# Optimization experiments

Measured on AMD Instinct MI355X. Metric: run time of the kernel, lower is better.

## Reference

```python
import jax, jax.numpy as jnp
import numpy as np

B, N, M, D = 8, 1024, 2048, 1024


def setup_inputs() -> dict:
    key = jax.random.key(0)
    k1, k2, k3 = jax.random.split(key, 3)
    text_features = jax.random.normal(k1, (B, N, D), dtype=jnp.float32)
    audio_features = jax.random.normal(k2, (B, M, D), dtype=jnp.float32)
    sigma = jnp.ones((1,), dtype=jnp.float32)  # learnable bandwidth, initial_sigma=1.0
    # audio lengths in [M//4, M) so no softmax row is fully masked
    audio_lengths = jnp.maximum(
        jax.random.randint(k3, (B,), 0, M), M // 4
    ).astype(jnp.int32)
    return {
        "text_features": text_features,
        "audio_features": audio_features,
        "sigma": sigma,
        "audio_lengths": audio_lengths,
    }


def reference(text_features, audio_features, sigma, audio_lengths):
    b, n, d = text_features.shape
    m = audio_features.shape[1]
    s = jnp.abs(sigma[0]) + 1e-8

    # QK^T / sqrt(d)  -> (B, N, M)
    scores = jnp.einsum("bnd,bmd->bnm", text_features, audio_features) / jnp.sqrt(
        jnp.float32(d)
    )

    # Gaussian relative positional bias: -|i/N - j/M|^2 / (2 sigma^2)
    text_pos = jnp.arange(n, dtype=jnp.float32) / n    # (N,)
    audio_pos = jnp.arange(m, dtype=jnp.float32) / m   # (M,)
    d_rel = jnp.abs(text_pos[:, None] - audio_pos[None, :])  # (N, M)
    scores = scores - d_rel**2 / (2.0 * s * s)

    # mask padded audio positions per batch element
    valid = jnp.arange(m)[None, :] < audio_lengths[:, None]  # (B, M) bool
    scores = jnp.where(valid[:, None, :], scores, -jnp.inf)

    attention_weights = jax.nn.softmax(scores, axis=-1)  # (B, N, M)
    enhanced = jnp.einsum("bnm,bmd->bnd", attention_weights, audio_features)
    return enhanced, attention_weights
```

## Files before the change

kernel.cpp:

```cpp
#include <hip/hip_runtime.h>
#include <hip/hip_bf16.h>

#define BB 8
#define NN 1024
#define MM 2048
#define DD 1024

typedef __attribute__((ext_vector_type(8))) __bf16 bfrag8;
typedef __attribute__((ext_vector_type(4))) float ffrag4;

__device__ __forceinline__ unsigned short f2bf(float f) {
  union { float f; unsigned u; } x; x.f = f;
  unsigned r = x.u + 0x7FFFu + ((x.u >> 16) & 1u);
  return (unsigned short)(r >> 16);
}

__device__ __forceinline__ void gload_lds16(const unsigned short* g, unsigned short* l) {
  __builtin_amdgcn_global_load_lds(
      (const __attribute__((address_space(1))) void*)g,
      (__attribute__((address_space(3))) void*)l, 16, 0, 0);
}

#define SCHED0() __builtin_amdgcn_sched_barrier(0)
#define P_PRE()  do { SCHED0(); __builtin_amdgcn_s_barrier();                 \
                      asm volatile("s_waitcnt lgkmcnt(0)" ::: "memory");      \
                      SCHED0(); __builtin_amdgcn_s_setprio(1); } while (0)
#define P_POST() do { __builtin_amdgcn_s_setprio(0); SCHED0();                \
                      __builtin_amdgcn_s_barrier(); } while (0)

#define MFMA16x16x32 __builtin_amdgcn_mfma_f32_16x16x32_bf16

__device__ __forceinline__ void stage_half(const unsigned short* gbase, int ldk,
                                           unsigned short* ldst,
                                           int w, int r0, int slog) {
  const unsigned short* g = gbase + (size_t)(w * 8 + r0) * ldk + slog;
  gload_lds16(g, ldst + w * 512);
  gload_lds16(g + (size_t)64 * ldk, ldst + 4096 + w * 512);
}

#define TSTR 68
__global__ __launch_bounds__(256) void ta_prep(
    const float* __restrict__ Q, const float* __restrict__ V,
    unsigned short* __restrict__ Qbf,
    unsigned short* __restrict__ Kbf, unsigned short* __restrict__ VT,
    float* __restrict__ sums)
{
  __shared__ unsigned short Tls[64 * TSTR];
  const int bid = blockIdx.x;
  const int t = threadIdx.x;

  if (bid < 4096) {
    int tt = bid * 256 + t;
    const float4* src = reinterpret_cast<const float4*>(Q) + tt * 2;
    float4 a = src[0], b = src[1];
    ushort4 lo = { f2bf(a.x), f2bf(a.y), f2bf(a.z), f2bf(a.w) };
    ushort4 hi = { f2bf(b.x), f2bf(b.y), f2bf(b.z), f2bf(b.w) };
    ushort4* dst = reinterpret_cast<ushort4*>(Qbf) + tt * 2;
    dst[0] = lo; dst[1] = hi;
  } else if (bid < 8192) {
    const int id = bid - 4096;
    const int dt = id & 15;
    const int mt = (id >> 4) & 31;
    const int b  = id >> 9;

    const float* Vb = V + (size_t)b * MM * DD + (size_t)(mt * 64) * DD + dt * 64;
#pragma unroll
    for (int it = 0; it < 4; ++it) {
      int slot = t + 256 * it;
      int row  = slot >> 4;
      int c4   = slot & 15;
      float4 a = *reinterpret_cast<const float4*>(Vb + (size_t)row * DD + c4 * 4);
      ushort4 h = { f2bf(a.x), f2bf(a.y), f2bf(a.z), f2bf(a.w) };
      *reinterpret_cast<ushort4*>(&Tls[row * TSTR + c4 * 4]) = h;
    }
    __syncthreads();

    unsigned short* Kb = Kbf + (size_t)b * MM * DD + (size_t)(mt * 64) * DD + dt * 64;
    unsigned short* Vt = VT  + (size_t)b * DD * MM + (size_t)(dt * 64) * MM + mt * 64;
#pragma unroll
    for (int it = 0; it < 4; ++it) {
      int slot = t + 256 * it;
      int row  = slot >> 4;
      int c4   = slot & 15;
      *reinterpret_cast<ushort4*>(Kb + (size_t)row * DD + c4 * 4) =
          *reinterpret_cast<const ushort4*>(&Tls[row * TSTR + c4 * 4]);
      ushort4 tv = { Tls[(c4 * 4 + 0) * TSTR + row],
                     Tls[(c4 * 4 + 1) * TSTR + row],
                     Tls[(c4 * 4 + 2) * TSTR + row],
                     Tls[(c4 * 4 + 3) * TSTR + row] };
      *reinterpret_cast<ushort4*>(Vt + (size_t)row * MM + c4 * 4) = tv;
    }
  } else {
    int tt = (bid - 8192) * 256 + t;
    sums[tt] = 0.0f;
  }
}

__global__ void ta_zero(float* __restrict__ sums) {
  int t = blockIdx.x * 256 + threadIdx.x;
  if (t < BB * NN) sums[t] = 0.0f;
}

__global__ __launch_bounds__(512, 2) void ta_gemm1x(
    const unsigned short* __restrict__ Q,
    const unsigned short* __restrict__ K,
    const float* __restrict__ sigma,
    const int* __restrict__ lens,
    unsigned short* __restrict__ Ebf,
    float* __restrict__ rowsum)
{
  const int bj = blockIdx.x, bi = blockIdx.y, b = blockIdx.z;
  const int t = threadIdx.x;
  const int lane = t & 63, w = t >> 6;
  const int wr = w >> 2, wc = w & 3;
  __shared__ unsigned short S[65536];

  const unsigned short* Qb = Q + (size_t)b * NN * DD + (size_t)(bi * 256) * DD;
  const unsigned short* Kb = K + (size_t)b * MM * DD + (size_t)(bj * 256) * DD;

  const int r  = lane & 15, qd = lane >> 4;
  const int r0 = (lane >> 3) & 7;
  const int slog = ((lane & 7) ^ r0) << 3;
  const int cs0 = ((qd)     ^ (r & 7)) << 3;
  const int cs1 = ((4 + qd) ^ (r & 7)) << 3;

  ffrag4 acc[8][4] = {};

  {
    unsigned short* T0 = &S[0];
    stage_half(Qb,                        DD, T0,          w, r0, slog);
    stage_half(Qb + (size_t)128 * DD,     DD, T0 + 8192,   w, r0, slog);
    stage_half(Kb,                        DD, T0 + 16384,  w, r0, slog);
    stage_half(Kb + (size_t)128 * DD,     DD, T0 + 24576,  w, r0, slog);
    unsigned short* T1 = &S[32768];
    stage_half(Qb + 64,                    DD, T1,          w, r0, slog);
    stage_half(Qb + (size_t)128 * DD + 64, DD, T1 + 8192,   w, r0, slog);
    stage_half(Kb + 64,                    DD, T1 + 16384,  w, r0, slog);
    stage_half(Kb + (size_t)128 * DD + 64, DD, T1 + 24576,  w, r0, slog);
    asm volatile("s_waitcnt vmcnt(8)" ::: "memory");
    __builtin_amdgcn_s_barrier();
  }

  for (int kt = 0; kt < 16; ++kt) {
    const int p = kt & 1;
    unsigned short* Ab = &S[p * 32768 + wr * 8192];
    unsigned short* Bb = &S[p * 32768 + 16384 + (wc >> 1) * 8192];
    const int brb = (wc & 1) * 64;
    bfrag8 af[4][2], bf0[2][2], bf1[2][2];

#pragma unroll
    for (int mi = 0; mi < 4; ++mi) {
      const unsigned short* a = &Ab[(mi * 16 + r) * 64];
      af[mi][0] = *reinterpret_cast<const bfrag8*>(a + cs0);
      af[mi][1] = *reinterpret_cast<const bfrag8*>(a + cs1);
    }
#pragma unroll
    for (int jj = 0; jj < 2; ++jj) {
      const unsigned short* bp = &Bb[(brb + jj * 16 + r) * 64];
      bf0[jj][0] = *reinterpret_cast<const bfrag8*>(bp + cs0);
      bf0[jj][1] = *reinterpret_cast<const bfrag8*>(bp + cs1);
    }
    P_PRE();
#pragma unroll
    for (int mi = 0; mi < 4; ++mi)
#pragma unroll
      for (int jj = 0; jj < 2; ++jj) {
        acc[mi][jj] = MFMA16x16x32(af[mi][0], bf0[jj][0], acc[mi][jj], 0, 0, 0);
        acc[mi][jj] = MFMA16x16x32(af[mi][1], bf0[jj][1], acc[mi][jj], 0, 0, 0);
      }
    P_POST();

#pragma unroll
    for (int jj = 0; jj < 2; ++jj) {
      const unsigned short* bp = &Bb[(brb + (2 + jj) * 16 + r) * 64];
      bf1[jj][0] = *reinterpret_cast<const bfrag8*>(bp + cs0);
      bf1[jj][1] = *reinterpret_cast<const bfrag8*>(bp + cs1);
    }
    P_PRE();
#pragma unroll
    for (int mi = 0; mi < 4; ++mi)
#pragma unroll
      for (int jj = 0; jj < 2; ++jj) {
        acc[mi][2 + jj] = MFMA16x16x32(af[mi][0], bf1[jj][0], acc[mi][2 + jj], 0, 0, 0);
        acc[mi][2 + jj] = MFMA16x16x32(af[mi][1], bf1[jj][1], acc[mi][2 + jj], 0, 0, 0);
      }
    P_POST();

#pragma unroll
    for (int mi = 0; mi < 4; ++mi) {
      const unsigned short* a = &Ab[((mi + 4) * 16 + r) * 64];
      af[mi][0] = *reinterpret_cast<const bfrag8*>(a + cs0);
      af[mi][1] = *reinterpret_cast<const bfrag8*>(a + cs1);
    }
    if (kt + 2 < 16) {
      unsigned short* Dst = &S[p * 32768 + 16384];
      stage_half(Kb + (kt + 2) * 64,                    DD, Dst,        w, r0, slog);
      stage_half(Kb + (size_t)128 * DD + (kt + 2) * 64, DD, Dst + 8192, w, r0, slog);
    }
    P_PRE();
#pragma unroll
    for (int mi = 0; mi < 4; ++mi)
#pragma unroll
      for (int jj = 0; jj < 2; ++jj) {
        acc[4 + mi][2 + jj] = MFMA16x16x32(af[mi][0], bf1[jj][0], acc[4 + mi][2 + jj], 0, 0, 0);
        acc[4 + mi][2 + jj] = MFMA16x16x32(af[mi][1], bf1[jj][1], acc[4 + mi][2 + jj], 0, 0, 0);
      }
    P_POST();

    if (kt + 2 < 16) {
      unsigned short* Dst = &S[p * 32768];
      stage_half(Qb + (kt + 2) * 64,                    DD, Dst,        w, r0, slog);
      stage_half(Qb + (size_t)128 * DD + (kt + 2) * 64, DD, Dst + 8192, w, r0, slog);
    }
    P_PRE();
#pragma unroll
    for (int mi = 0; mi < 4; ++mi)
#pragma unroll
      for (int jj = 0; jj < 2; ++jj) {
        acc[4 + mi][jj] = MFMA16x16x32(af[mi][0], bf0[jj][0], acc[4 + mi][jj], 0, 0, 0);
        acc[4 + mi][jj] = MFMA16x16x32(af[mi][1], bf0[jj][1], acc[4 + mi][jj], 0, 0, 0);
      }
    __builtin_amdgcn_s_setprio(0);
    SCHED0();
    if (kt + 2 < 16)      { asm volatile("s_waitcnt vmcnt(8)" ::: "memory"); }
    else if (kt + 1 < 16) { asm volatile("s_waitcnt vmcnt(0)" ::: "memory"); }
    __builtin_amdgcn_s_barrier();
  }

  const float sg = fabsf(sigma[0]) + 1e-8f;
  const float inv2s2 = 1.0f / (2.0f * sg * sg);
  const int len = lens[b];
  unsigned short* Erow = Ebf + (size_t)b * NN * MM;
  float* sums = rowsum + (size_t)b * NN;
  const int ibase = bi * 256 + wr * 128;
  const int jbase = bj * 256 + wc * 64;
#pragma unroll
  for (int mi = 0; mi < 8; ++mi) {
#pragma unroll
    for (int v = 0; v < 4; ++v) {
      int i = ibase + mi * 16 + qd * 4 + v;
      float psum = 0.0f;
#pragma unroll
      for (int nj = 0; nj < 4; ++nj) {
        int j = jbase + nj * 16 + r;
        float e = 0.0f;
        if (j < len) {
          float dr = (float)i * (1.0f / (float)NN) - (float)j * (1.0f / (float)MM);
          float sc = acc[mi][nj][v] * 0.03125f - dr * dr * inv2s2;
          e = __expf(fminf(sc, 30.0f));
        }
        psum += e;
        Erow[(size_t)i * MM + j] = f2bf(e);
      }
      psum += __shfl_xor(psum, 1);
      psum += __shfl_xor(psum, 2);
      psum += __shfl_xor(psum, 4);
      psum += __shfl_xor(psum, 8);
      if (r == 0) atomicAdd(&sums[i], psum);
    }
  }
}

__global__ __launch_bounds__(512, 2) void ta_gemm2x(
    const unsigned short* __restrict__ E,
    const unsigned short* __restrict__ VT,
    const float* __restrict__ rowsum,
    float* __restrict__ O,
    float* __restrict__ attn)
{
  const int bd = blockIdx.x, bi = blockIdx.y, b = blockIdx.z;
  const int t = threadIdx.x;
  const int lane = t & 63, w = t >> 6;
  const int wr = w >> 2, wc = w & 3;
  __shared__ unsigned short S[49152];

  const unsigned short* Eb = E  + (size_t)b * NN * MM + (size_t)(bi * 128) * MM;
  const unsigned short* Vb = VT + (size_t)b * DD * MM + (size_t)(bd * 256) * MM;

  const int r  = lane & 15, qd = lane >> 4;
  const int r0 = (lane >> 3) & 7;
  const int slog = ((lane & 7) ^ r0) << 3;
  const int cs0 = ((qd)     ^ (r & 7)) << 3;
  const int cs1 = ((4 + qd) ^ (r & 7)) << 3;

  ffrag4 acc[4][4] = {};

  {
    stage_half(Eb,                        MM, &S[0],     w, r0, slog);
    stage_half(Vb,                        MM, &S[8192],  w, r0, slog);
    stage_half(Vb + (size_t)128 * MM,     MM, &S[16384], w, r0, slog);
    stage_half(Eb + 64,                    MM, &S[24576],         w, r0, slog);
    stage_half(Vb + 64,                    MM, &S[24576 + 8192],  w, r0, slog);
    stage_half(Vb + (size_t)128 * MM + 64, MM, &S[24576 + 16384], w, r0, slog);
    asm volatile("s_waitcnt vmcnt(6)" ::: "memory");
    __builtin_amdgcn_s_barrier();
  }

  for (int kt = 0; kt < 32; ++kt) {
    const int p = kt & 1;
    unsigned short* Ab = &S[p * 24576];
    unsigned short* Bb = &S[p * 24576 + 8192 + (wc >> 1) * 8192];
    const int arb = wr * 64;
    const int brb = (wc & 1) * 64;
    bfrag8 af[2][2], bf0[2][2], bf1[2][2];

#pragma unroll
    for (int mi = 0; mi < 2; ++mi) {
      const unsigned short* a = &Ab[(arb + mi * 16 + r) * 64];
      af[mi][0] = *reinterpret_cast<const bfrag8*>(a + cs0);
      af[mi][1] = *reinterpret_cast<const bfrag8*>(a + cs1);
    }
#pragma unroll
    for (int jj = 0; jj < 2; ++jj) {
      const unsigned short* bp = &Bb[(brb + jj * 16 + r) * 64];
      bf0[jj][0] = *reinterpret_cast<const bfrag8*>(bp + cs0);
      bf0[jj][1] = *reinterpret_cast<const bfrag8*>(bp + cs1);
    }
    P_PRE();
#pragma unroll
    for (int mi = 0; mi < 2; ++mi)
#pragma unroll
      for (int jj = 0; jj < 2; ++jj) {
        acc[mi][jj] = MFMA16x16x32(af[mi][0], bf0[jj][0], acc[mi][jj], 0, 0, 0);
        acc[mi][jj] = MFMA16x16x32(af[mi][1], bf0[jj][1], acc[mi][jj], 0, 0, 0);
      }
    P_POST();

#pragma unroll
    for (int jj = 0; jj < 2; ++jj) {
      const unsigned short* bp = &Bb[(brb + (2 + jj) * 16 + r) * 64];
      bf1[jj][0] = *reinterpret_cast<const bfrag8*>(bp + cs0);
      bf1[jj][1] = *reinterpret_cast<const bfrag8*>(bp + cs1);
    }
    P_PRE();
#pragma unroll
    for (int mi = 0; mi < 2; ++mi)
#pragma unroll
      for (int jj = 0; jj < 2; ++jj) {
        acc[mi][2 + jj] = MFMA16x16x32(af[mi][0], bf1[jj][0], acc[mi][2 + jj], 0, 0, 0);
        acc[mi][2 + jj] = MFMA16x16x32(af[mi][1], bf1[jj][1], acc[mi][2 + jj], 0, 0, 0);
      }
    P_POST();

#pragma unroll
    for (int mi = 0; mi < 2; ++mi) {
      const unsigned short* a = &Ab[(arb + (mi + 2) * 16 + r) * 64];
      af[mi][0] = *reinterpret_cast<const bfrag8*>(a + cs0);
      af[mi][1] = *reinterpret_cast<const bfrag8*>(a + cs1);
    }
    if (kt + 2 < 32) {
      unsigned short* Dst = &S[p * 24576 + 8192];
      stage_half(Vb + (kt + 2) * 64,                    MM, Dst,        w, r0, slog);
      stage_half(Vb + (size_t)128 * MM + (kt + 2) * 64, MM, Dst + 8192, w, r0, slog);
    }
    P_PRE();
#pragma unroll
    for (int mi = 0; mi < 2; ++mi)
#pragma unroll
      for (int jj = 0; jj < 2; ++jj) {
        acc[2 + mi][2 + jj] = MFMA16x16x32(af[mi][0], bf1[jj][0], acc[2 + mi][2 + jj], 0, 0, 0);
        acc[2 + mi][2 + jj] = MFMA16x16x32(af[mi][1], bf1[jj][1], acc[2 + mi][2 + jj], 0, 0, 0);
      }
    P_POST();

    if (kt + 2 < 32) {
      stage_half(Eb + (kt + 2) * 64, MM, &S[p * 24576], w, r0, slog);
    }
    P_PRE();
#pragma unroll
    for (int mi = 0; mi < 2; ++mi)
#pragma unroll
      for (int jj = 0; jj < 2; ++jj) {
        acc[2 + mi][jj] = MFMA16x16x32(af[mi][0], bf0[jj][0], acc[2 + mi][jj], 0, 0, 0);
        acc[2 + mi][jj] = MFMA16x16x32(af[mi][1], bf0[jj][1], acc[2 + mi][jj], 0, 0, 0);
      }
    __builtin_amdgcn_s_setprio(0);
    SCHED0();
    if (kt + 2 < 32)      { asm volatile("s_waitcnt vmcnt(6)" ::: "memory"); }
    else if (kt + 1 < 32) { asm volatile("s_waitcnt vmcnt(0)" ::: "memory"); }
    __builtin_amdgcn_s_barrier();
  }

  float* Ob = O + (size_t)b * NN * DD;
  const float* rs = rowsum + (size_t)b * NN;
  const int ibase = bi * 128 + wr * 64;
  const int dbase = bd * 256 + wc * 64;
#pragma unroll
  for (int mi = 0; mi < 4; ++mi) {
#pragma unroll
    for (int v = 0; v < 4; ++v) {
      int i = ibase + mi * 16 + qd * 4 + v;
      float inv = 1.0f / fmaxf(rs[i], 1e-30f);
#pragma unroll
      for (int nj = 0; nj < 4; ++nj) {
        int d = dbase + nj * 16 + r;
        Ob[(size_t)i * DD + d] = acc[mi][nj][v] * inv;
      }
    }
  }

  {
    float* attnB = attn + ((size_t)b * NN + bi * 128) * MM + bd * 512;
    const unsigned short* Eslice = Eb + bd * 512;
#pragma unroll
    for (int it = 0; it < 16; ++it) {
      int c = t + it * 512;
      int row = c >> 6;
      int col = (c & 63) * 8;
      float inv = 1.0f / fmaxf(rs[bi * 128 + row], 1e-30f);
      uint4 x = *reinterpret_cast<const uint4*>(Eslice + (size_t)row * MM + col);
      unsigned u[4] = { x.x, x.y, x.z, x.w };
      float o[8];
#pragma unroll
      for (int k = 0; k < 4; ++k) {
        union { unsigned u; float f; } lo, hi;
        lo.u = u[k] << 16; hi.u = u[k] & 0xFFFF0000u;
        o[2 * k]     = lo.f * inv;
        o[2 * k + 1] = hi.f * inv;
      }
      float4* dst = reinterpret_cast<float4*>(attnB + (size_t)row * MM + col);
      float4 f0 = { o[0], o[1], o[2], o[3] };
      float4 f1 = { o[4], o[5], o[6], o[7] };
      dst[0] = f0; dst[1] = f1;
    }
  }
}

#define LDA 40
__global__ __launch_bounds__(256) void tb_gemm1e(
    const float* __restrict__ Q, const float* __restrict__ K,
    const float* __restrict__ sigma, const int* __restrict__ lens,
    float* __restrict__ attn, float* __restrict__ rowsum)
{
  const int bj = blockIdx.x, bi = blockIdx.y, b = blockIdx.z;
  const int t = threadIdx.x;
  const int lane = t & 63;
  const int w = t >> 6;
  const int wi = w >> 1, wj = w & 1;
  __shared__ unsigned short Als[128 * LDA];
  __shared__ unsigned short Bls[128 * LDA];
  const float* Qb = Q + (size_t)b * NN * DD + (size_t)(bi * 128) * DD;
  const float* Kb = K + (size_t)b * MM * DD + (size_t)(bj * 128) * DD;
  ffrag4 acc[4][4] = {};
  const int r = lane & 15;
  const int koff = (lane >> 4) * 8;
  for (int k0 = 0; k0 < DD; k0 += 32) {
#pragma unroll
    for (int it = 0; it < 4; ++it) {
      int slot = t + 256 * it;
      int row = slot >> 3, c4 = slot & 7;
      float4 qa = *reinterpret_cast<const float4*>(Qb + (size_t)row * DD + k0 + c4 * 4);
      float4 ka = *reinterpret_cast<const float4*>(Kb + (size_t)row * DD + k0 + c4 * 4);
      ushort4 qh = { f2bf(qa.x), f2bf(qa.y), f2bf(qa.z), f2bf(qa.w) };
      ushort4 kh = { f2bf(ka.x), f2bf(ka.y), f2bf(ka.z), f2bf(ka.w) };
      *reinterpret_cast<ushort4*>(&Als[row * LDA + c4 * 4]) = qh;
      *reinterpret_cast<ushort4*>(&Bls[row * LDA + c4 * 4]) = kh;
    }
    __syncthreads();
    bfrag8 af[4], bf[4];
#pragma unroll
    for (int ti = 0; ti < 4; ++ti)
      af[ti] = *reinterpret_cast<const bfrag8*>(&Als[(wi * 64 + ti * 16 + r) * LDA + koff]);
#pragma unroll
    for (int tj = 0; tj < 4; ++tj)
      bf[tj] = *reinterpret_cast<const bfrag8*>(&Bls[(wj * 64 + tj * 16 + r) * LDA + koff]);
#pragma unroll
    for (int ti = 0; ti < 4; ++ti)
#pragma unroll
      for (int tj = 0; tj < 4; ++tj)
        acc[ti][tj] = MFMA16x16x32(af[ti], bf[tj], acc[ti][tj], 0, 0, 0);
    __syncthreads();
  }
  const float s = fabsf(sigma[0]) + 1e-8f;
  const float inv2s2 = 1.0f / (2.0f * s * s);
  const int len = lens[b];
  float* Prow = attn + (size_t)b * NN * MM;
  float* sums = rowsum + (size_t)b * NN;
  const int ibase = bi * 128 + wi * 64;
  const int jbase = bj * 128 + wj * 64;
  const int quad = lane >> 4;
#pragma unroll
  for (int ti = 0; ti < 4; ++ti) {
#pragma unroll
    for (int v = 0; v < 4; ++v) {
      int i = ibase + ti * 16 + quad * 4 + v;
      float psum = 0.0f;
#pragma unroll
      for (int tj = 0; tj < 4; ++tj) {
        int j = jbase + tj * 16 + r;
        float e = 0.0f;
        if (j < len) {
          float dr = (float)i * (1.0f / (float)NN) - (float)j * (1.0f / (float)MM);
          float sc = acc[ti][tj][v] * 0.03125f - dr * dr * inv2s2;
          e = __expf(fminf(sc, 30.0f));
        }
        psum += e;
        Prow[(size_t)i * MM + j] = e;
      }
      psum += __shfl_xor(psum, 1);
      psum += __shfl_xor(psum, 2);
      psum += __shfl_xor(psum, 4);
      psum += __shfl_xor(psum, 8);
      if (r == 0) atomicAdd(&sums[i], psum);
    }
  }
}

__global__ __launch_bounds__(256) void tb_norm(float* __restrict__ attn,
                                               const float* __restrict__ sums) {
  int t = blockIdx.x * 256 + threadIdx.x;
  int row = t >> 9;
  const float inv = 1.0f / fmaxf(sums[row], 1e-30f);
  float4* p = reinterpret_cast<float4*>(attn) + t;
  float4 x = *p;
  x.x *= inv; x.y *= inv; x.z *= inv; x.w *= inv;
  *p = x;
}

__global__ __launch_bounds__(256) void tb_gemm2(
    const float* __restrict__ P, const float* __restrict__ V, float* __restrict__ O)
{
  const int bd = blockIdx.x, bi = blockIdx.y, b = blockIdx.z;
  const int t = threadIdx.x;
  const int lane = t & 63;
  const int w = t >> 6;
  const int wi = w >> 1, wj = w & 1;
  __shared__ unsigned short Pls[128 * LDA];
  __shared__ unsigned short Vls[128 * LDA];
  const float* Pb = P + (size_t)b * NN * MM + (size_t)(bi * 128) * MM;
  const float* Vb = V + (size_t)b * MM * DD + bd * 128;
  ffrag4 acc[4][4] = {};
  const int r = lane & 15;
  const int koff = (lane >> 4) * 8;
  const int vd = t & 127;
  const int vmb = (t >> 7) * 16;
  for (int k0 = 0; k0 < MM; k0 += 32) {
#pragma unroll
    for (int it = 0; it < 4; ++it) {
      int slot = t + 256 * it;
      int row = slot >> 3, c4 = slot & 7;
      float4 pa = *reinterpret_cast<const float4*>(Pb + (size_t)row * MM + k0 + c4 * 4);
      ushort4 ph = { f2bf(pa.x), f2bf(pa.y), f2bf(pa.z), f2bf(pa.w) };
      *reinterpret_cast<ushort4*>(&Pls[row * LDA + c4 * 4]) = ph;
    }
    union { unsigned short h[16]; uint4 q[2]; } hv;
#pragma unroll
    for (int i = 0; i < 16; ++i)
      hv.h[i] = f2bf(Vb[(size_t)(k0 + vmb + i) * DD + vd]);
    *reinterpret_cast<uint4*>(&Vls[vd * LDA + vmb]) = hv.q[0];
    *reinterpret_cast<uint4*>(&Vls[vd * LDA + vmb + 8]) = hv.q[1];
    __syncthreads();
    bfrag8 af[4], bf[4];
#pragma unroll
    for (int ti = 0; ti < 4; ++ti)
      af[ti] = *reinterpret_cast<const bfrag8*>(&Pls[(wi * 64 + ti * 16 + r) * LDA + koff]);
#pragma unroll
    for (int tj = 0; tj < 4; ++tj)
      bf[tj] = *reinterpret_cast<const bfrag8*>(&Vls[(wj * 64 + tj * 16 + r) * LDA + koff]);
#pragma unroll
    for (int ti = 0; ti < 4; ++ti)
#pragma unroll
      for (int tj = 0; tj < 4; ++tj)
        acc[ti][tj] = MFMA16x16x32(af[ti], bf[tj], acc[ti][tj], 0, 0, 0);
    __syncthreads();
  }
  float* Ob = O + (size_t)b * NN * DD;
  const int ibase = bi * 128 + wi * 64;
  const int dbase = bd * 128 + wj * 64;
#pragma unroll
  for (int ti = 0; ti < 4; ++ti) {
#pragma unroll
    for (int tj = 0; tj < 4; ++tj) {
      int d = dbase + tj * 16 + r;
#pragma unroll
      for (int v = 0; v < 4; ++v) {
        int i = ibase + ti * 16 + (lane >> 4) * 4 + v;
        Ob[(size_t)i * DD + d] = acc[ti][tj][v];
      }
    }
  }
}

extern "C" void kernel_launch(void* const* d_in, const int* in_sizes, int n_in,
                              void* d_out, int out_size, void* d_ws, size_t ws_size,
                              hipStream_t stream) {
  const float* text  = (const float*)d_in[0];
  const float* audio = (const float*)d_in[1];
  const float* sigma = (const float*)d_in[2];
  const int*   lens  = (const int*)d_in[3];

  float* out = (float*)d_out;
  float* enhanced = out;
  float* attn = out + (size_t)BB * NN * DD;

  const size_t QBF  = (size_t)BB * NN * DD * 2;
  const size_t KBF  = (size_t)BB * MM * DD * 2;
  const size_t VTB  = (size_t)BB * DD * MM * 2;
  const size_t EBF  = (size_t)BB * NN * MM * 2;
  const size_t offQ = 65536;
  const size_t offK = offQ + QBF;
  const size_t offV = offK + KBF;
  const size_t offE = offV + VTB;
  const size_t need = offE + EBF;

  float* rowsum = (float*)d_ws;

  if (ws_size >= need) {
    unsigned short* Qbf = (unsigned short*)((char*)d_ws + offQ);
    unsigned short* Kbf = (unsigned short*)((char*)d_ws + offK);
    unsigned short* VT  = (unsigned short*)((char*)d_ws + offV);
    unsigned short* Ebf = (unsigned short*)((char*)d_ws + offE);

    ta_prep<<<dim3(8224), 256, 0, stream>>>(text, audio, Qbf, Kbf, VT, rowsum);
    ta_gemm1x<<<dim3(MM / 256, NN / 256, BB), 512, 0, stream>>>(Qbf, Kbf, sigma, lens, Ebf, rowsum);
    ta_gemm2x<<<dim3(DD / 256, NN / 128, BB), 512, 0, stream>>>(Ebf, VT, rowsum, enhanced, attn);
  } else {
    ta_zero<<<dim3((BB * NN + 255) / 256), 256, 0, stream>>>(rowsum);
    tb_gemm1e<<<dim3(MM / 128, NN / 128, BB), 256, 0, stream>>>(text, audio, sigma, lens, attn, rowsum);
    tb_norm<<<dim3(BB * NN * MM / 4 / 256), 256, 0, stream>>>(attn, rowsum);
    tb_gemm2<<<dim3(DD / 128, NN / 128, BB), 256, 0, stream>>>(attn, audio, enhanced);
  }
}
```

Measured before the change: 276.6 us.

## Interleave attention-weight writeback into PV loop, remap blocks, trim barriers

```diff
diff --git a/kernel.cpp b/kernel.cpp
--- a/kernel.cpp
+++ b/kernel.cpp
@@ -22,12 +22,6 @@
 }
 
 #define SCHED0() __builtin_amdgcn_sched_barrier(0)
-#define P_PRE()  do { SCHED0(); __builtin_amdgcn_s_barrier();                 \
-                      asm volatile("s_waitcnt lgkmcnt(0)" ::: "memory");      \
-                      SCHED0(); __builtin_amdgcn_s_setprio(1); } while (0)
-#define P_POST() do { __builtin_amdgcn_s_setprio(0); SCHED0();                \
-                      __builtin_amdgcn_s_barrier(); } while (0)
-
 #define MFMA16x16x32 __builtin_amdgcn_mfma_f32_16x16x32_bf16
 
 __device__ __forceinline__ void stage_half(const unsigned short* gbase, int ldk,
@@ -109,7 +103,10 @@
     unsigned short* __restrict__ Ebf,
     float* __restrict__ rowsum)
 {
-  const int bj = blockIdx.x, bi = blockIdx.y, b = blockIdx.z;
+  const int lin = blockIdx.x + 8 * (blockIdx.y + 4 * blockIdx.z);
+  const int wid = (lin & 7) * 32 + (lin >> 3);
+  const int bj = wid & 7, bi = (wid >> 3) & 3, b = wid >> 5;
+
   const int t = threadIdx.x;
   const int lane = t & 63, w = t >> 6;
   const int wr = w >> 2, wc = w & 3;
@@ -141,6 +138,7 @@
     __builtin_amdgcn_s_barrier();
   }
 
+#pragma unroll 2
   for (int kt = 0; kt < 16; ++kt) {
     const int p = kt & 1;
     unsigned short* Ab = &S[p * 32768 + wr * 8192];
@@ -160,7 +158,8 @@
       bf0[jj][0] = *reinterpret_cast<const bfrag8*>(bp + cs0);
       bf0[jj][1] = *reinterpret_cast<const bfrag8*>(bp + cs1);
     }
-    P_PRE();
+    asm volatile("s_waitcnt lgkmcnt(0)" ::: "memory");
+    SCHED0(); __builtin_amdgcn_s_setprio(1);
 #pragma unroll
     for (int mi = 0; mi < 4; ++mi)
 #pragma unroll
@@ -168,7 +167,7 @@
         acc[mi][jj] = MFMA16x16x32(af[mi][0], bf0[jj][0], acc[mi][jj], 0, 0, 0);
         acc[mi][jj] = MFMA16x16x32(af[mi][1], bf0[jj][1], acc[mi][jj], 0, 0, 0);
       }
-    P_POST();
+    __builtin_amdgcn_s_setprio(0); SCHED0();
 
 #pragma unroll
     for (int jj = 0; jj < 2; ++jj) {
@@ -176,7 +175,9 @@
       bf1[jj][0] = *reinterpret_cast<const bfrag8*>(bp + cs0);
       bf1[jj][1] = *reinterpret_cast<const bfrag8*>(bp + cs1);
     }
-    P_PRE();
+    asm volatile("s_waitcnt lgkmcnt(0)" ::: "memory");
+    SCHED0(); __builtin_amdgcn_s_barrier();
+    __builtin_amdgcn_s_setprio(1);
 #pragma unroll
     for (int mi = 0; mi < 4; ++mi)
 #pragma unroll
@@ -184,7 +185,7 @@
         acc[mi][2 + jj] = MFMA16x16x32(af[mi][0], bf1[jj][0], acc[mi][2 + jj], 0, 0, 0);
         acc[mi][2 + jj] = MFMA16x16x32(af[mi][1], bf1[jj][1], acc[mi][2 + jj], 0, 0, 0);
       }
-    P_POST();
+    __builtin_amdgcn_s_setprio(0); SCHED0();
 
 #pragma unroll
     for (int mi = 0; mi < 4; ++mi) {
@@ -197,7 +198,9 @@
       stage_half(Kb + (kt + 2) * 64,                    DD, Dst,        w, r0, slog);
       stage_half(Kb + (size_t)128 * DD + (kt + 2) * 64, DD, Dst + 8192, w, r0, slog);
     }
-    P_PRE();
+    asm volatile("s_waitcnt lgkmcnt(0)" ::: "memory");
+    SCHED0(); __builtin_amdgcn_s_barrier();
+    __builtin_amdgcn_s_setprio(1);
 #pragma unroll
     for (int mi = 0; mi < 4; ++mi)
 #pragma unroll
@@ -205,14 +208,14 @@
         acc[4 + mi][2 + jj] = MFMA16x16x32(af[mi][0], bf1[jj][0], acc[4 + mi][2 + jj], 0, 0, 0);
         acc[4 + mi][2 + jj] = MFMA16x16x32(af[mi][1], bf1[jj][1], acc[4 + mi][2 + jj], 0, 0, 0);
       }
-    P_POST();
+    __builtin_amdgcn_s_setprio(0); SCHED0();
 
     if (kt + 2 < 16) {
       unsigned short* Dst = &S[p * 32768];
       stage_half(Qb + (kt + 2) * 64,                    DD, Dst,        w, r0, slog);
       stage_half(Qb + (size_t)128 * DD + (kt + 2) * 64, DD, Dst + 8192, w, r0, slog);
     }
-    P_PRE();
+    SCHED0(); __builtin_amdgcn_s_setprio(1);
 #pragma unroll
     for (int mi = 0; mi < 4; ++mi)
 #pragma unroll
@@ -220,8 +223,7 @@
         acc[4 + mi][jj] = MFMA16x16x32(af[mi][0], bf0[jj][0], acc[4 + mi][jj], 0, 0, 0);
         acc[4 + mi][jj] = MFMA16x16x32(af[mi][1], bf0[jj][1], acc[4 + mi][jj], 0, 0, 0);
       }
-    __builtin_amdgcn_s_setprio(0);
-    SCHED0();
+    __builtin_amdgcn_s_setprio(0); SCHED0();
     if (kt + 2 < 16)      { asm volatile("s_waitcnt vmcnt(8)" ::: "memory"); }
     else if (kt + 1 < 16) { asm volatile("s_waitcnt vmcnt(0)" ::: "memory"); }
     __builtin_amdgcn_s_barrier();
@@ -268,7 +270,10 @@
     float* __restrict__ O,
     float* __restrict__ attn)
 {
-  const int bd = blockIdx.x, bi = blockIdx.y, b = blockIdx.z;
+  const int lin = blockIdx.x + 4 * (blockIdx.y + 8 * blockIdx.z);
+  const int wid = (lin & 7) * 32 + (lin >> 3);
+  const int bd = wid & 3, bi = (wid >> 2) & 7, b = wid >> 5;
+
   const int t = threadIdx.x;
   const int lane = t & 63, w = t >> 6;
   const int wr = w >> 2, wc = w & 3;
@@ -284,6 +289,14 @@
   const int cs1 = ((4 + qd) ^ (r & 7)) << 3;
 
   ffrag4 acc[4][4] = {};
+
+  const float* rsB = rowsum + (size_t)b * NN;
+  const float* rsT = rsB + bi * 128;
+  float* attnB = attn + ((size_t)b * NN + bi * 128) * MM + bd * 512;
+  const unsigned short* Eslice = Eb + bd * 512;
+  uint4 ax = {0, 0, 0, 0};
+  float ainv = 0.0f;
+  int arow = 0, acol = 0;
 
   {
     stage_half(Eb,                        MM, &S[0],     w, r0, slog);
@@ -296,93 +309,86 @@
     __builtin_amdgcn_s_barrier();
   }
 
+#pragma unroll 2
   for (int kt = 0; kt < 32; ++kt) {
     const int p = kt & 1;
     unsigned short* Ab = &S[p * 24576];
     unsigned short* Bb = &S[p * 24576 + 8192 + (wc >> 1) * 8192];
     const int arb = wr * 64;
     const int brb = (wc & 1) * 64;
-    bfrag8 af[2][2], bf0[2][2], bf1[2][2];
-
-#pragma unroll
-    for (int mi = 0; mi < 2; ++mi) {
+    bfrag8 af[4][2], bf[4][2];
+
+#pragma unroll
+    for (int mi = 0; mi < 4; ++mi) {
       const unsigned short* a = &Ab[(arb + mi * 16 + r) * 64];
       af[mi][0] = *reinterpret_cast<const bfrag8*>(a + cs0);
       af[mi][1] = *reinterpret_cast<const bfrag8*>(a + cs1);
     }
 #pragma unroll
-    for (int jj = 0; jj < 2; ++jj) {
-      const unsigned short* bp = &Bb[(brb + jj * 16 + r) * 64];
-      bf0[jj][0] = *reinterpret_cast<const bfrag8*>(bp + cs0);
-      bf0[jj][1] = *reinterpret_cast<const bfrag8*>(bp + cs1);
-    }
-    P_PRE();
+    for (int nj = 0; nj < 4; ++nj) {
+      const unsigned short* bp = &Bb[(brb + nj * 16 + r) * 64];
+      bf[nj][0] = *reinterpret_cast<const bfrag8*>(bp + cs0);
+      bf[nj][1] = *reinterpret_cast<const bfrag8*>(bp + cs1);
+    }
+
+    if ((kt & 1) == 0) {
+      int it = kt >> 1;
+      int c = t + it * 512;
+      arow = c >> 6;
+      acol = (c & 63) * 8;
+      ax = *reinterpret_cast<const uint4*>(Eslice + (size_t)arow * MM + acol);
+      ainv = 1.0f / fmaxf(rsT[arow], 1e-30f);
+    } else {
+      unsigned u[4] = { ax.x, ax.y, ax.z, ax.w };
+      float o[8];
+#pragma unroll
+      for (int k2 = 0; k2 < 4; ++k2) {
+        union { unsigned u; float f; } lo, hi;
+        lo.u = u[k2] << 16; hi.u = u[k2] & 0xFFFF0000u;
+        o[2 * k2]     = lo.f * ainv;
+        o[2 * k2 + 1] = hi.f * ainv;
+      }
+      float4* dst = reinterpret_cast<float4*>(attnB + (size_t)arow * MM + acol);
+      float4 f0 = { o[0], o[1], o[2], o[3] };
+      float4 f1 = { o[4], o[5], o[6], o[7] };
+      dst[0] = f0; dst[1] = f1;
+    }
+
+    asm volatile("s_waitcnt lgkmcnt(0)" ::: "memory");
+    SCHED0(); __builtin_amdgcn_s_barrier();
+    __builtin_amdgcn_s_setprio(1);
 #pragma unroll
     for (int mi = 0; mi < 2; ++mi)
 #pragma unroll
-      for (int jj = 0; jj < 2; ++jj) {
-        acc[mi][jj] = MFMA16x16x32(af[mi][0], bf0[jj][0], acc[mi][jj], 0, 0, 0);
-        acc[mi][jj] = MFMA16x16x32(af[mi][1], bf0[jj][1], acc[mi][jj], 0, 0, 0);
-      }
-    P_POST();
-
-#pragma unroll
-    for (int jj = 0; jj < 2; ++jj) {
-      const unsigned short* bp = &Bb[(brb + (2 + jj) * 16 + r) * 64];
-      bf1[jj][0] = *reinterpret_cast<const bfrag8*>(bp + cs0);
-      bf1[jj][1] = *reinterpret_cast<const bfrag8*>(bp + cs1);
-    }
-    P_PRE();
-#pragma unroll
-    for (int mi = 0; mi < 2; ++mi)
-#pragma unroll
-      for (int jj = 0; jj < 2; ++jj) {
-        acc[mi][2 + jj] = MFMA16x16x32(af[mi][0], bf1[jj][0], acc[mi][2 + jj], 0, 0, 0);
-        acc[mi][2 + jj] = MFMA16x16x32(af[mi][1], bf1[jj][1], acc[mi][2 + jj], 0, 0, 0);
-      }
-    P_POST();
-
-#pragma unroll
-    for (int mi = 0; mi < 2; ++mi) {
-      const unsigned short* a = &Ab[(arb + (mi + 2) * 16 + r) * 64];
-      af[mi][0] = *reinterpret_cast<const bfrag8*>(a + cs0);
-      af[mi][1] = *reinterpret_cast<const bfrag8*>(a + cs1);
-    }
+      for (int nj = 0; nj < 4; ++nj) {
+        acc[mi][nj] = MFMA16x16x32(af[mi][0], bf[nj][0], acc[mi][nj], 0, 0, 0);
+        acc[mi][nj] = MFMA16x16x32(af[mi][1], bf[nj][1], acc[mi][nj], 0, 0, 0);
+      }
+    __builtin_amdgcn_s_setprio(0); SCHED0();
+
     if (kt + 2 < 32) {
-      unsigned short* Dst = &S[p * 24576 + 8192];
-      stage_half(Vb + (kt + 2) * 64,                    MM, Dst,        w, r0, slog);
-      stage_half(Vb + (size_t)128 * MM + (kt + 2) * 64, MM, Dst + 8192, w, r0, slog);
-    }
-    P_PRE();
-#pragma unroll
-    for (int mi = 0; mi < 2; ++mi)
-#pragma unroll
-      for (int jj = 0; jj < 2; ++jj) {
-        acc[2 + mi][2 + jj] = MFMA16x16x32(af[mi][0], bf1[jj][0], acc[2 + mi][2 + jj], 0, 0, 0);
-        acc[2 + mi][2 + jj] = MFMA16x16x32(af[mi][1], bf1[jj][1], acc[2 + mi][2 + jj], 0, 0, 0);
-      }
-    P_POST();
-
-    if (kt + 2 < 32) {
-      stage_half(Eb + (kt + 2) * 64, MM, &S[p * 24576], w, r0, slog);
-    }
-    P_PRE();
-#pragma unroll
-    for (int mi = 0; mi < 2; ++mi)
-#pragma unroll
-      for (int jj = 0; jj < 2; ++jj) {
-        acc[2 + mi][jj] = MFMA16x16x32(af[mi][0], bf0[jj][0], acc[2 + mi][jj], 0, 0, 0);
-        acc[2 + mi][jj] = MFMA16x16x32(af[mi][1], bf0[jj][1], acc[2 + mi][jj], 0, 0, 0);
-      }
-    __builtin_amdgcn_s_setprio(0);
-    SCHED0();
+      unsigned short* Dst = &S[p * 24576];
+      stage_half(Eb + (kt + 2) * 64,                    MM, Dst,         w, r0, slog);
+      stage_half(Vb + (kt + 2) * 64,                    MM, Dst + 8192,  w, r0, slog);
+      stage_half(Vb + (size_t)128 * MM + (kt + 2) * 64, MM, Dst + 16384, w, r0, slog);
+    }
+
+    SCHED0(); __builtin_amdgcn_s_setprio(1);
+#pragma unroll
+    for (int mi = 2; mi < 4; ++mi)
+#pragma unroll
+      for (int nj = 0; nj < 4; ++nj) {
+        acc[mi][nj] = MFMA16x16x32(af[mi][0], bf[nj][0], acc[mi][nj], 0, 0, 0);
+        acc[mi][nj] = MFMA16x16x32(af[mi][1], bf[nj][1], acc[mi][nj], 0, 0, 0);
+      }
+    __builtin_amdgcn_s_setprio(0); SCHED0();
+
     if (kt + 2 < 32)      { asm volatile("s_waitcnt vmcnt(6)" ::: "memory"); }
     else if (kt + 1 < 32) { asm volatile("s_waitcnt vmcnt(0)" ::: "memory"); }
     __builtin_amdgcn_s_barrier();
   }
 
   float* Ob = O + (size_t)b * NN * DD;
-  const float* rs = rowsum + (size_t)b * NN;
   const int ibase = bi * 128 + wr * 64;
   const int dbase = bd * 256 + wc * 64;
 #pragma unroll
@@ -390,38 +396,12 @@
 #pragma unroll
     for (int v = 0; v < 4; ++v) {
       int i = ibase + mi * 16 + qd * 4 + v;
-      float inv = 1.0f / fmaxf(rs[i], 1e-30f);
+      float inv = 1.0f / fmaxf(rsB[i], 1e-30f);
 #pragma unroll
       for (int nj = 0; nj < 4; ++nj) {
         int d = dbase + nj * 16 + r;
         Ob[(size_t)i * DD + d] = acc[mi][nj][v] * inv;
       }
-    }
-  }
-
-  {
-    float* attnB = attn + ((size_t)b * NN + bi * 128) * MM + bd * 512;
-    const unsigned short* Eslice = Eb + bd * 512;
-#pragma unroll
-    for (int it = 0; it < 16; ++it) {
-      int c = t + it * 512;
-      int row = c >> 6;
-      int col = (c & 63) * 8;
-      float inv = 1.0f / fmaxf(rs[bi * 128 + row], 1e-30f);
-      uint4 x = *reinterpret_cast<const uint4*>(Eslice + (size_t)row * MM + col);
-      unsigned u[4] = { x.x, x.y, x.z, x.w };
-      float o[8];
-#pragma unroll
-      for (int k = 0; k < 4; ++k) {
-        union { unsigned u; float f; } lo, hi;
-        lo.u = u[k] << 16; hi.u = u[k] & 0xFFFF0000u;
-        o[2 * k]     = lo.f * inv;
-        o[2 * k + 1] = hi.f * inv;
-      }
-      float4* dst = reinterpret_cast<float4*>(attnB + (size_t)row * MM + col);
-      float4 f0 = { o[0], o[1], o[2], o[3] };
-      float4 f1 = { o[4], o[5], o[6], o[7] };
-      dst[0] = f0; dst[1] = f1;
     }
   }
 }
```

New measurement: 263.6 us. 4.7% less time.
